# Kernel tuning notes

Measured on AMD Instinct MI355X. Metric: run time of the kernel, lower is better.

Reference implementation:

```python
import jax, jax.numpy as jnp
import numpy as np

N, E, D = 50000, 600000, 128
LN_EPS = 1e-5


def setup_inputs() -> dict:
    key = jax.random.key(0)
    ks = jax.random.split(key, 7)
    s = 1.0 / np.sqrt(D)
    x = jax.random.normal(ks[0], (N, D), dtype=jnp.float32)
    edge_index = jax.random.randint(ks[1], (2, E), 0, N, dtype=jnp.int32)
    Wq = jax.random.normal(ks[2], (D, D), dtype=jnp.float32) * s
    Wk = jax.random.normal(ks[3], (D, D), dtype=jnp.float32) * s
    Wv = jax.random.normal(ks[4], (D, D), dtype=jnp.float32) * s
    Wo = jax.random.normal(ks[5], (D, D), dtype=jnp.float32) * s
    bo = jnp.zeros((D,), dtype=jnp.float32)
    gamma = jnp.ones((D,), dtype=jnp.float32)
    beta = jnp.zeros((D,), dtype=jnp.float32)
    return {"x": x, "edge_index": edge_index, "Wq": Wq, "Wk": Wk,
            "Wv": Wv, "Wo": Wo, "bo": bo, "gamma": gamma, "beta": beta}


def reference(x, edge_index, Wq, Wk, Wv, Wo, bo, gamma, beta):
    src, dst = edge_index[0], edge_index[1]
    # gather endpoint features, project (torch Linear: y = x @ W.T)
    q = x[dst] @ Wq.T                      # [E, D]
    k = x[src] @ Wk.T                      # [E, D]
    v = x[src] @ Wv.T                      # [E, D]
    logits = jnp.sum(q * k, axis=-1, keepdims=True) / np.sqrt(D)  # [E, 1]
    msg = jax.nn.sigmoid(logits) * v       # [E, D]
    agg = jax.ops.segment_sum(msg, dst, num_segments=N)  # scatter-add -> [N, D]
    out = agg @ Wo.T + bo
    h = x + out
    # LayerNorm over last dim
    mu = jnp.mean(h, axis=-1, keepdims=True)
    var = jnp.mean(jnp.square(h - mu), axis=-1, keepdims=True)
    return (h - mu) * jax.lax.rsqrt(var + LN_EPS) * gamma + beta
```

## Files before the change

kernel.cpp:

```cpp
#include <hip/hip_runtime.h>
#include <math.h>


#define BM 64
#define QSCALE -0.08838834764831845f

typedef __attribute__((ext_vector_type(8))) short bfrag;
typedef __attribute__((ext_vector_type(4))) float f32x4;

__device__ __forceinline__ short f2bf(float f) {
    union { float f; unsigned u; } v; v.f = f;
    unsigned r = v.u + 0x7FFFu + ((v.u >> 16) & 1u);
    return (short)(r >> 16);
}
__device__ __forceinline__ float bf2f(short h) {
    union { unsigned u; float f; } v;
    v.u = ((unsigned)(unsigned short)h) << 16;
    return v.f;
}
__device__ __forceinline__ float klo(unsigned w) {
    union { unsigned u; float f; } v; v.u = w << 16; return v.f;
}
__device__ __forceinline__ float vhi(unsigned w) {
    union { unsigned u; float f; } v; v.u = w & 0xffff0000u; return v.f;
}

#define SWZ(x, pat) __int_as_float(__builtin_amdgcn_ds_swizzle(__float_as_int(x), pat))

__global__ __launch_bounds__(256) void zero_prep(
    const float* __restrict__ Wq, const float* __restrict__ Wk,
    const float* __restrict__ Wv, const float* __restrict__ Wo,
    short* __restrict__ whi, short* __restrict__ wlo,
    int* __restrict__ hist, int N)
{
    int g = blockIdx.x * 256 + threadIdx.x;
    if (g < N) hist[g] = 0;
    if (g < 65536) {
        const float* Ws[4] = {Wq, Wk, Wv, Wo};
        float f = Ws[g >> 14][g & 16383];
        short h = f2bf(f);
        short l = f2bf(f - bf2f(h));
        whi[g] = h; wlo[g] = l;
    }
}

__global__ __launch_bounds__(256) void qkv_mfma(
    const float* __restrict__ x,
    const short* __restrict__ whi, const short* __restrict__ wlo,
    float* __restrict__ Q, unsigned short* __restrict__ KV16, int N)
{
    __shared__ short xs_hi[64][136];
    __shared__ short xs_lo[64][136];

    const int tid = threadIdx.x;
    const int row0 = blockIdx.x * BM;

    #pragma unroll
    for (int i = 0; i < 8; ++i) {
        int idx = tid + 256 * i;
        int r = idx >> 5;
        int c4 = idx & 31;
        int gr = row0 + r;
        float4 val = make_float4(0.f, 0.f, 0.f, 0.f);
        if (gr < N) val = ((const float4*)(x + (size_t)gr * 128))[c4];
        short4 h, l;
        h.x = f2bf(val.x); l.x = f2bf(val.x - bf2f(h.x));
        h.y = f2bf(val.y); l.y = f2bf(val.y - bf2f(h.y));
        h.z = f2bf(val.z); l.z = f2bf(val.z - bf2f(h.z));
        h.w = f2bf(val.w); l.w = f2bf(val.w - bf2f(h.w));
        *((short4*)&xs_hi[r][c4 * 4]) = h;
        *((short4*)&xs_lo[r][c4 * 4]) = l;
    }
    __syncthreads();

    const int wid  = tid >> 6;
    const int lane = tid & 63;
    const int n16  = lane & 15;
    const int quad = lane >> 4;

    #pragma unroll 1
    for (int mat = 0; mat < 3; ++mat) {
        const short* __restrict__ WH = whi + mat * 16384;
        const short* __restrict__ WL = wlo + mat * 16384;
        const f32x4 zero = {0.f, 0.f, 0.f, 0.f};
        f32x4 acc[4][2];
        #pragma unroll
        for (int t = 0; t < 4; ++t) { acc[t][0] = zero; acc[t][1] = zero; }

        #pragma unroll
        for (int kc = 0; kc < 4; ++kc) {
            int k0 = kc * 32 + quad * 8;
            bfrag ah[4], al[4], bh[2], bl[2];
            #pragma unroll
            for (int t = 0; t < 4; ++t) {
                ah[t] = *((const bfrag*)&xs_hi[t * 16 + n16][k0]);
                al[t] = *((const bfrag*)&xs_lo[t * 16 + n16][k0]);
            }
            #pragma unroll
            for (int c = 0; c < 2; ++c) {
                int wr = (wid * 2 + c) * 16 + n16;
                bh[c] = *((const bfrag*)(WH + wr * 128 + k0));
                bl[c] = *((const bfrag*)(WL + wr * 128 + k0));
            }
            #pragma unroll
            for (int t = 0; t < 4; ++t)
                #pragma unroll
                for (int c = 0; c < 2; ++c) {
                    acc[t][c] = __builtin_amdgcn_mfma_f32_16x16x32_bf16(ah[t], bh[c], acc[t][c], 0, 0, 0);
                    acc[t][c] = __builtin_amdgcn_mfma_f32_16x16x32_bf16(al[t], bh[c], acc[t][c], 0, 0, 0);
                    acc[t][c] = __builtin_amdgcn_mfma_f32_16x16x32_bf16(ah[t], bl[c], acc[t][c], 0, 0, 0);
                }
        }
        #pragma unroll
        for (int t = 0; t < 4; ++t)
            #pragma unroll
            for (int r = 0; r < 4; ++r) {
                int grow = row0 + t * 16 + quad * 4 + r;
                if (grow < N) {
                    int c0 = (wid * 2 + 0) * 16 + n16;
                    int c1 = (wid * 2 + 1) * 16 + n16;
                    if (mat == 0) {
                        Q[(size_t)grow * 128 + c0] = acc[t][0][r] * QSCALE;
                        Q[(size_t)grow * 128 + c1] = acc[t][1][r] * QSCALE;
                    } else {
                        size_t base = (size_t)grow * 256 + (mat - 1);
                        KV16[base + 2 * c0] = (unsigned short)f2bf(acc[t][0][r]);
                        KV16[base + 2 * c1] = (unsigned short)f2bf(acc[t][1][r]);
                    }
                }
            }
    }
}

__global__ __launch_bounds__(256) void hist_kernel(
    const int* __restrict__ ei, int* __restrict__ hist, int E)
{
    int e = blockIdx.x * blockDim.x + threadIdx.x;
    if (e < E) atomicAdd(&hist[ei[E + e]], 1);
}

#define SCAN_TPB 256
#define SCAN_EPT 4

__global__ __launch_bounds__(SCAN_TPB) void scan_partial(
    const int* __restrict__ hist, int* __restrict__ offs,
    int* __restrict__ blockSums, int N)
{
    __shared__ int sdata[SCAN_TPB];
    int b = blockIdx.x;
    int t = threadIdx.x;
    int base = b * SCAN_TPB * SCAN_EPT + t * SCAN_EPT;
    int v[SCAN_EPT];
    int tot = 0;
    #pragma unroll
    for (int j = 0; j < SCAN_EPT; ++j) {
        int idx = base + j;
        v[j] = (idx < N) ? hist[idx] : 0;
        tot += v[j];
    }
    sdata[t] = tot;
    __syncthreads();
    for (int off = 1; off < SCAN_TPB; off <<= 1) {
        int xv = (t >= off) ? sdata[t - off] : 0;
        __syncthreads();
        sdata[t] += xv;
        __syncthreads();
    }
    int run = sdata[t] - tot;
    #pragma unroll
    for (int j = 0; j < SCAN_EPT; ++j) {
        int idx = base + j;
        if (idx < N) offs[idx] = run;
        run += v[j];
    }
    if (t == SCAN_TPB - 1) blockSums[b] = sdata[t];
}

__global__ __launch_bounds__(256) void scan_blocksums(int* __restrict__ blockSums, int nb)
{
    __shared__ int sdata[256];
    int t = threadIdx.x;
    int orig = (t < nb) ? blockSums[t] : 0;
    sdata[t] = orig;
    __syncthreads();
    for (int off = 1; off < 256; off <<= 1) {
        int xv = (t >= off) ? sdata[t - off] : 0;
        __syncthreads();
        sdata[t] += xv;
        __syncthreads();
    }
    if (t < nb) blockSums[t] = sdata[t] - orig;
}

__global__ __launch_bounds__(256) void scan_add(
    int* __restrict__ offs, int* __restrict__ starts,
    const int* __restrict__ blockSums, int N)
{
    int idx = blockIdx.x * blockDim.x + threadIdx.x;
    if (idx < N) {
        int vv = offs[idx] + blockSums[idx >> 10];
        offs[idx] = vv;
        starts[idx] = vv;
    }
}

__global__ __launch_bounds__(256) void scatter_kernel(
    const int* __restrict__ ei, int* __restrict__ offs,
    int* __restrict__ ssrc, int E)
{
    int e = blockIdx.x * blockDim.x + threadIdx.x;
    if (e < E) {
        int d = ei[E + e];
        int pos = atomicAdd(&offs[d], 1);
        ssrc[pos] = ei[e];
    }
}

__global__ __launch_bounds__(256) void node_agg(
    const int* __restrict__ ssrc,
    const int* __restrict__ starts,
    const int* __restrict__ endoffs,
    const float* __restrict__ Q, const unsigned short* __restrict__ KV16,
    float* __restrict__ agg, int N)
{
    int node = blockIdx.x * 4 + (threadIdx.x >> 6);
    if (node >= N) return;
    int lane = threadIdx.x & 63;
    int eg   = lane >> 4;
    int sl   = lane & 15;
    int start = starts[node];
    int end   = endoffs[node];

    const float4 q0 = *((const float4*)(Q + (size_t)node * 128 + sl * 8));
    const float4 q1 = *((const float4*)(Q + (size_t)node * 128 + sl * 8 + 4));

    float a0 = 0.f, a1 = 0.f, a2 = 0.f, a3 = 0.f;
    float a4 = 0.f, a5 = 0.f, a6 = 0.f, a7 = 0.f;

    const unsigned short* kvbase = KV16 + sl * 16;

    for (int i = start; i < end; i += 8) {
        int i0 = i + eg;
        int i1 = i + 4 + eg;
        int ok0 = (i0 < end);
        int ok1 = (i1 < end);
        i0 = ok0 ? i0 : (end - 1);
        i1 = ok1 ? i1 : (end - 1);
        int s0 = ssrc[i0];
        int s1 = ssrc[i1];
        const unsigned short* kp0 = kvbase + ((size_t)s0 << 8);
        const unsigned short* kp1 = kvbase + ((size_t)s1 << 8);
        uint4 wa0 = *((const uint4*)kp0);
        uint4 wa1 = *((const uint4*)(kp0 + 8));
        uint4 wb0 = *((const uint4*)kp1);
        uint4 wb1 = *((const uint4*)(kp1 + 8));

        float p0, p1;
        p0 = q0.x * klo(wa0.x);
        p0 = fmaf(q0.y, klo(wa0.y), p0);
        p0 = fmaf(q0.z, klo(wa0.z), p0);
        p0 = fmaf(q0.w, klo(wa0.w), p0);
        p0 = fmaf(q1.x, klo(wa1.x), p0);
        p0 = fmaf(q1.y, klo(wa1.y), p0);
        p0 = fmaf(q1.z, klo(wa1.z), p0);
        p0 = fmaf(q1.w, klo(wa1.w), p0);
        p1 = q0.x * klo(wb0.x);
        p1 = fmaf(q0.y, klo(wb0.y), p1);
        p1 = fmaf(q0.z, klo(wb0.z), p1);
        p1 = fmaf(q0.w, klo(wb0.w), p1);
        p1 = fmaf(q1.x, klo(wb1.x), p1);
        p1 = fmaf(q1.y, klo(wb1.y), p1);
        p1 = fmaf(q1.z, klo(wb1.z), p1);
        p1 = fmaf(q1.w, klo(wb1.w), p1);

        p0 += SWZ(p0, 0x041F); p1 += SWZ(p1, 0x041F);
        p0 += SWZ(p0, 0x081F); p1 += SWZ(p1, 0x081F);
        p0 += SWZ(p0, 0x101F); p1 += SWZ(p1, 0x101F);
        p0 += SWZ(p0, 0x201F); p1 += SWZ(p1, 0x201F);

        float c0 = __builtin_amdgcn_rcpf(1.f + __expf(p0));
        float c1 = __builtin_amdgcn_rcpf(1.f + __expf(p1));
        if (!ok0) c0 = 0.f;
        if (!ok1) c1 = 0.f;

        a0 = fmaf(c0, vhi(wa0.x), a0); a0 = fmaf(c1, vhi(wb0.x), a0);
        a1 = fmaf(c0, vhi(wa0.y), a1); a1 = fmaf(c1, vhi(wb0.y), a1);
        a2 = fmaf(c0, vhi(wa0.z), a2); a2 = fmaf(c1, vhi(wb0.z), a2);
        a3 = fmaf(c0, vhi(wa0.w), a3); a3 = fmaf(c1, vhi(wb0.w), a3);
        a4 = fmaf(c0, vhi(wa1.x), a4); a4 = fmaf(c1, vhi(wb1.x), a4);
        a5 = fmaf(c0, vhi(wa1.y), a5); a5 = fmaf(c1, vhi(wb1.y), a5);
        a6 = fmaf(c0, vhi(wa1.z), a6); a6 = fmaf(c1, vhi(wb1.z), a6);
        a7 = fmaf(c0, vhi(wa1.w), a7); a7 = fmaf(c1, vhi(wb1.w), a7);
    }

    a0 += SWZ(a0, 0x401F); a1 += SWZ(a1, 0x401F);
    a2 += SWZ(a2, 0x401F); a3 += SWZ(a3, 0x401F);
    a4 += SWZ(a4, 0x401F); a5 += SWZ(a5, 0x401F);
    a6 += SWZ(a6, 0x401F); a7 += SWZ(a7, 0x401F);
    a0 += __shfl_xor(a0, 32); a1 += __shfl_xor(a1, 32);
    a2 += __shfl_xor(a2, 32); a3 += __shfl_xor(a3, 32);
    a4 += __shfl_xor(a4, 32); a5 += __shfl_xor(a5, 32);
    a6 += __shfl_xor(a6, 32); a7 += __shfl_xor(a7, 32);

    if (eg == 0) {
        *((float4*)(agg + (size_t)node * 128 + sl * 8))     = make_float4(a0, a1, a2, a3);
        *((float4*)(agg + (size_t)node * 128 + sl * 8 + 4)) = make_float4(a4, a5, a6, a7);
    }
}

__global__ __launch_bounds__(256) void out_ln_mfma(
    const float* __restrict__ agg,
    const short* __restrict__ whi, const short* __restrict__ wlo,
    const float* __restrict__ bo, const float* __restrict__ x,
    const float* __restrict__ gamma, const float* __restrict__ beta,
    float* __restrict__ out, int N)
{
    __shared__ __align__(16) char smem[64 * 136 * 2 * 2];
    short (*xs_hi)[136] = (short(*)[136])smem;
    short (*xs_lo)[136] = (short(*)[136])(smem + 64 * 136 * 2);
    float (*hs)[132]    = (float(*)[132])smem;

    const int tid = threadIdx.x;
    const int row0 = blockIdx.x * BM;

    #pragma unroll
    for (int i = 0; i < 8; ++i) {
        int idx = tid + 256 * i;
        int r = idx >> 5;
        int c4 = idx & 31;
        int gr = row0 + r;
        float4 val = make_float4(0.f, 0.f, 0.f, 0.f);
        if (gr < N) val = ((const float4*)(agg + (size_t)gr * 128))[c4];
        short4 h, l;
        h.x = f2bf(val.x); l.x = f2bf(val.x - bf2f(h.x));
        h.y = f2bf(val.y); l.y = f2bf(val.y - bf2f(h.y));
        h.z = f2bf(val.z); l.z = f2bf(val.z - bf2f(h.z));
        h.w = f2bf(val.w); l.w = f2bf(val.w - bf2f(h.w));
        *((short4*)&xs_hi[r][c4 * 4]) = h;
        *((short4*)&xs_lo[r][c4 * 4]) = l;
    }
    __syncthreads();

    const int wid  = tid >> 6;
    const int lane = tid & 63;
    const int n16  = lane & 15;
    const int quad = lane >> 4;
    const short* __restrict__ WH = whi + 3 * 16384;
    const short* __restrict__ WL = wlo + 3 * 16384;

    const f32x4 zero = {0.f, 0.f, 0.f, 0.f};
    f32x4 acc[4][2];
    #pragma unroll
    for (int t = 0; t < 4; ++t) { acc[t][0] = zero; acc[t][1] = zero; }

    #pragma unroll
    for (int kc = 0; kc < 4; ++kc) {
        int k0 = kc * 32 + quad * 8;
        bfrag ah[4], al[4], bh[2], bl[2];
        #pragma unroll
        for (int t = 0; t < 4; ++t) {
            ah[t] = *((const bfrag*)&xs_hi[t * 16 + n16][k0]);
            al[t] = *((const bfrag*)&xs_lo[t * 16 + n16][k0]);
        }
        #pragma unroll
        for (int c = 0; c < 2; ++c) {
            int wr = (wid * 2 + c) * 16 + n16;
            bh[c] = *((const bfrag*)(WH + wr * 128 + k0));
            bl[c] = *((const bfrag*)(WL + wr * 128 + k0));
        }
        #pragma unroll
        for (int t = 0; t < 4; ++t)
            #pragma unroll
            for (int c = 0; c < 2; ++c) {
                acc[t][c] = __builtin_amdgcn_mfma_f32_16x16x32_bf16(ah[t], bh[c], acc[t][c], 0, 0, 0);
                acc[t][c] = __builtin_amdgcn_mfma_f32_16x16x32_bf16(al[t], bh[c], acc[t][c], 0, 0, 0);
                acc[t][c] = __builtin_amdgcn_mfma_f32_16x16x32_bf16(ah[t], bl[c], acc[t][c], 0, 0, 0);
            }
    }
    __syncthreads();

    #pragma unroll
    for (int t = 0; t < 4; ++t)
        #pragma unroll
        for (int r = 0; r < 4; ++r) {
            hs[t * 16 + quad * 4 + r][(wid * 2 + 0) * 16 + n16] = acc[t][0][r];
            hs[t * 16 + quad * 4 + r][(wid * 2 + 1) * 16 + n16] = acc[t][1][r];
        }
    __syncthreads();

    {
        int r = tid >> 2;
        int qd = tid & 3;
        int gr = row0 + r;
        float sum = 0.f, sq = 0.f;
        #pragma unroll
        for (int c = 0; c < 32; c += 4) {
            float4 g4 = *((float4*)&hs[r][qd * 32 + c]);
            float4 b4 = *((const float4*)(bo + qd * 32 + c));
            float4 x4 = make_float4(0.f, 0.f, 0.f, 0.f);
            if (gr < N) x4 = *((const float4*)(x + (size_t)gr * 128 + qd * 32 + c));
            float4 h = make_float4(g4.x + b4.x + x4.x, g4.y + b4.y + x4.y,
                                   g4.z + b4.z + x4.z, g4.w + b4.w + x4.w);
            *((float4*)&hs[r][qd * 32 + c]) = h;
            sum += h.x + h.y + h.z + h.w;
            sq += h.x * h.x + h.y * h.y + h.z * h.z + h.w * h.w;
        }
        sum += __shfl_xor(sum, 1); sum += __shfl_xor(sum, 2);
        sq  += __shfl_xor(sq, 1);  sq  += __shfl_xor(sq, 2);
        float mu = sum * (1.f / 128.f);
        float var = sq * (1.f / 128.f) - mu * mu;
        float rs = rsqrtf(var + 1e-5f);
        if (gr < N) {
            #pragma unroll
            for (int c = 0; c < 32; c += 4) {
                float4 h = *((float4*)&hs[r][qd * 32 + c]);
                float4 g = *((const float4*)(gamma + qd * 32 + c));
                float4 b = *((const float4*)(beta + qd * 32 + c));
                float4 o = make_float4((h.x - mu) * rs * g.x + b.x,
                                       (h.y - mu) * rs * g.y + b.y,
                                       (h.z - mu) * rs * g.z + b.z,
                                       (h.w - mu) * rs * g.w + b.w);
                *((float4*)(out + (size_t)gr * 128 + qd * 32 + c)) = o;
            }
        }
    }
}

extern "C" void kernel_launch(void* const* d_in, const int* in_sizes, int n_in,
                              void* d_out, int out_size, void* d_ws, size_t ws_size,
                              hipStream_t stream) {
    const float* x     = (const float*)d_in[0];
    const int*   ei    = (const int*)d_in[1];
    const float* Wq    = (const float*)d_in[2];
    const float* Wk    = (const float*)d_in[3];
    const float* Wv    = (const float*)d_in[4];
    const float* Wo    = (const float*)d_in[5];
    const float* bo    = (const float*)d_in[6];
    const float* gamma = (const float*)d_in[7];
    const float* beta  = (const float*)d_in[8];
    const int N = in_sizes[0] / 128;
    const int E = in_sizes[1] / 2;
    const size_t ND = (size_t)N * 128;

    float* ws  = (float*)d_ws;
    float* Q   = ws;
    unsigned short* KV16 = (unsigned short*)(Q + ND);
    float* agg = (float*)(KV16 + 2 * ND);
    int* hist      = (int*)(agg + ND);
    int* offs      = hist + N;
    int* starts    = offs + N;
    int* blockSums = starts + N;
    int* ssrc      = blockSums + 256;
    short* whi     = (short*)(ssrc + E);
    short* wlo     = whi + 4 * 16384;

    const int gzp = ((N > 65536 ? N : 65536) + 255) / 256;
    zero_prep<<<gzp, 256, 0, stream>>>(Wq, Wk, Wv, Wo, whi, wlo, hist, N);

    hist_kernel<<<(E + 255) / 256, 256, 0, stream>>>(ei, hist, E);
    const int nScanBlocks = (N + SCAN_TPB * SCAN_EPT - 1) / (SCAN_TPB * SCAN_EPT);
    scan_partial<<<nScanBlocks, SCAN_TPB, 0, stream>>>(hist, offs, blockSums, N);
    scan_blocksums<<<1, 256, 0, stream>>>(blockSums, nScanBlocks);
    scan_add<<<(N + 255) / 256, 256, 0, stream>>>(offs, starts, blockSums, N);
    scatter_kernel<<<(E + 255) / 256, 256, 0, stream>>>(ei, offs, ssrc, E);

    const int gq = (N + BM - 1) / BM;
    qkv_mfma<<<gq, 256, 0, stream>>>(x, whi, wlo, Q, KV16, N);

    node_agg<<<(N + 3) / 4, 256, 0, stream>>>(ssrc, starts, offs, Q, KV16, agg, N);

    out_ln_mfma<<<gq, 256, 0, stream>>>(agg, whi, wlo, bo, x, gamma, beta,
                                        (float*)d_out, N);
}
```

Measured before the change: 280.8 us.

## Store Q in bf16, fuse block-sum scan, prefetch next edge batch in aggregation

Result: faster. 268.2 us (-4.5%).

```diff
diff --git a/kernel.cpp b/kernel.cpp
--- a/kernel.cpp
+++ b/kernel.cpp
@@ -47,7 +47,7 @@
 __global__ __launch_bounds__(256) void qkv_mfma(
     const float* __restrict__ x,
     const short* __restrict__ whi, const short* __restrict__ wlo,
-    float* __restrict__ Q, unsigned short* __restrict__ KV16, int N)
+    unsigned short* __restrict__ Q16, unsigned short* __restrict__ KV16, int N)
 {
     __shared__ short xs_hi[64][136];
     __shared__ short xs_lo[64][136];
@@ -120,8 +120,8 @@
                     int c0 = (wid * 2 + 0) * 16 + n16;
                     int c1 = (wid * 2 + 1) * 16 + n16;
                     if (mat == 0) {
-                        Q[(size_t)grow * 128 + c0] = acc[t][0][r] * QSCALE;
-                        Q[(size_t)grow * 128 + c1] = acc[t][1][r] * QSCALE;
+                        Q16[(size_t)grow * 128 + c0] = (unsigned short)f2bf(acc[t][0][r] * QSCALE);
+                        Q16[(size_t)grow * 128 + c1] = (unsigned short)f2bf(acc[t][1][r] * QSCALE);
                     } else {
                         size_t base = (size_t)grow * 256 + (mat - 1);
                         KV16[base + 2 * c0] = (unsigned short)f2bf(acc[t][0][r]);
@@ -176,29 +176,27 @@
     if (t == SCAN_TPB - 1) blockSums[b] = sdata[t];
 }
 
-__global__ __launch_bounds__(256) void scan_blocksums(int* __restrict__ blockSums, int nb)
-{
-    __shared__ int sdata[256];
-    int t = threadIdx.x;
-    int orig = (t < nb) ? blockSums[t] : 0;
-    sdata[t] = orig;
-    __syncthreads();
-    for (int off = 1; off < 256; off <<= 1) {
-        int xv = (t >= off) ? sdata[t - off] : 0;
-        __syncthreads();
-        sdata[t] += xv;
-        __syncthreads();
-    }
-    if (t < nb) blockSums[t] = sdata[t] - orig;
-}
-
 __global__ __launch_bounds__(256) void scan_add(
     int* __restrict__ offs, int* __restrict__ starts,
-    const int* __restrict__ blockSums, int N)
-{
+    const int* __restrict__ blockSums, int N, int nb)
+{
+    __shared__ int bs[64];
+    int t = threadIdx.x;
+    if (t < 64) {
+        int v = (t < nb) ? blockSums[t] : 0;
+        #pragma unroll
+        for (int off = 1; off < 64; off <<= 1) {
+            int u = __shfl_up(v, off);
+            if (t >= off) v += u;
+        }
+        bs[t] = v;
+    }
+    __syncthreads();
     int idx = blockIdx.x * blockDim.x + threadIdx.x;
     if (idx < N) {
-        int vv = offs[idx] + blockSums[idx >> 10];
+        int blk = idx >> 10;
+        int pref = (blk == 0) ? 0 : bs[blk - 1];
+        int vv = offs[idx] + pref;
         offs[idx] = vv;
         starts[idx] = vv;
     }
@@ -220,7 +218,8 @@
     const int* __restrict__ ssrc,
     const int* __restrict__ starts,
     const int* __restrict__ endoffs,
-    const float* __restrict__ Q, const unsigned short* __restrict__ KV16,
+    const unsigned short* __restrict__ Q16,
+    const unsigned short* __restrict__ KV16,
     float* __restrict__ agg, int N)
 {
     int node = blockIdx.x * 4 + (threadIdx.x >> 6);
@@ -231,21 +230,27 @@
     int start = starts[node];
     int end   = endoffs[node];
 
-    const float4 q0 = *((const float4*)(Q + (size_t)node * 128 + sl * 8));
-    const float4 q1 = *((const float4*)(Q + (size_t)node * 128 + sl * 8 + 4));
+    if (start >= end) {
+        if (eg == 0) {
+            *((float4*)(agg + (size_t)node * 128 + sl * 8))     = make_float4(0.f, 0.f, 0.f, 0.f);
+            *((float4*)(agg + (size_t)node * 128 + sl * 8 + 4)) = make_float4(0.f, 0.f, 0.f, 0.f);
+        }
+        return;
+    }
+
+    bfrag qv = *((const bfrag*)(Q16 + (size_t)node * 128 + sl * 8));
+    float q0x = bf2f(qv[0]), q0y = bf2f(qv[1]), q0z = bf2f(qv[2]), q0w = bf2f(qv[3]);
+    float q1x = bf2f(qv[4]), q1y = bf2f(qv[5]), q1z = bf2f(qv[6]), q1w = bf2f(qv[7]);
 
     float a0 = 0.f, a1 = 0.f, a2 = 0.f, a3 = 0.f;
     float a4 = 0.f, a5 = 0.f, a6 = 0.f, a7 = 0.f;
 
     const unsigned short* kvbase = KV16 + sl * 16;
 
-    for (int i = start; i < end; i += 8) {
-        int i0 = i + eg;
-        int i1 = i + 4 + eg;
-        int ok0 = (i0 < end);
-        int ok1 = (i1 < end);
-        i0 = ok0 ? i0 : (end - 1);
-        i1 = ok1 ? i1 : (end - 1);
+    int i = start;
+    {
+        int i0 = i + eg;     i0 = (i0 < end) ? i0 : (end - 1);
+        int i1 = i + 4 + eg; i1 = (i1 < end) ? i1 : (end - 1);
         int s0 = ssrc[i0];
         int s1 = ssrc[i1];
         const unsigned short* kp0 = kvbase + ((size_t)s0 << 8);
@@ -255,42 +260,66 @@
         uint4 wb0 = *((const uint4*)kp1);
         uint4 wb1 = *((const uint4*)(kp1 + 8));
 
-        float p0, p1;
-        p0 = q0.x * klo(wa0.x);
-        p0 = fmaf(q0.y, klo(wa0.y), p0);
-        p0 = fmaf(q0.z, klo(wa0.z), p0);
-        p0 = fmaf(q0.w, klo(wa0.w), p0);
-        p0 = fmaf(q1.x, klo(wa1.x), p0);
-        p0 = fmaf(q1.y, klo(wa1.y), p0);
-        p0 = fmaf(q1.z, klo(wa1.z), p0);
-        p0 = fmaf(q1.w, klo(wa1.w), p0);
-        p1 = q0.x * klo(wb0.x);
-        p1 = fmaf(q0.y, klo(wb0.y), p1);
-        p1 = fmaf(q0.z, klo(wb0.z), p1);
-        p1 = fmaf(q0.w, klo(wb0.w), p1);
-        p1 = fmaf(q1.x, klo(wb1.x), p1);
-        p1 = fmaf(q1.y, klo(wb1.y), p1);
-        p1 = fmaf(q1.z, klo(wb1.z), p1);
-        p1 = fmaf(q1.w, klo(wb1.w), p1);
-
-        p0 += SWZ(p0, 0x041F); p1 += SWZ(p1, 0x041F);
-        p0 += SWZ(p0, 0x081F); p1 += SWZ(p1, 0x081F);
-        p0 += SWZ(p0, 0x101F); p1 += SWZ(p1, 0x101F);
-        p0 += SWZ(p0, 0x201F); p1 += SWZ(p1, 0x201F);
-
-        float c0 = __builtin_amdgcn_rcpf(1.f + __expf(p0));
-        float c1 = __builtin_amdgcn_rcpf(1.f + __expf(p1));
-        if (!ok0) c0 = 0.f;
-        if (!ok1) c1 = 0.f;
-
-        a0 = fmaf(c0, vhi(wa0.x), a0); a0 = fmaf(c1, vhi(wb0.x), a0);
-        a1 = fmaf(c0, vhi(wa0.y), a1); a1 = fmaf(c1, vhi(wb0.y), a1);
-        a2 = fmaf(c0, vhi(wa0.z), a2); a2 = fmaf(c1, vhi(wb0.z), a2);
-        a3 = fmaf(c0, vhi(wa0.w), a3); a3 = fmaf(c1, vhi(wb0.w), a3);
-        a4 = fmaf(c0, vhi(wa1.x), a4); a4 = fmaf(c1, vhi(wb1.x), a4);
-        a5 = fmaf(c0, vhi(wa1.y), a5); a5 = fmaf(c1, vhi(wb1.y), a5);
-        a6 = fmaf(c0, vhi(wa1.z), a6); a6 = fmaf(c1, vhi(wb1.z), a6);
-        a7 = fmaf(c0, vhi(wa1.w), a7); a7 = fmaf(c1, vhi(wb1.w), a7);
+        for (;;) {
+            bool more = (i + 8) < end;
+            uint4 na0, na1, nb0, nb1;
+            if (more) {
+                int j0 = i + 8 + eg;  j0 = (j0 < end) ? j0 : (end - 1);
+                int j1 = i + 12 + eg; j1 = (j1 < end) ? j1 : (end - 1);
+                int t0 = ssrc[j0];
+                int t1 = ssrc[j1];
+                const unsigned short* np0 = kvbase + ((size_t)t0 << 8);
+                const unsigned short* np1 = kvbase + ((size_t)t1 << 8);
+                na0 = *((const uint4*)np0);
+                na1 = *((const uint4*)(np0 + 8));
+                nb0 = *((const uint4*)np1);
+                nb1 = *((const uint4*)(np1 + 8));
+            }
+
+            int ok0 = ((i + eg) < end);
+            int ok1 = ((i + 4 + eg) < end);
+
+            float p0, p1;
+            p0 = q0x * klo(wa0.x);
+            p0 = fmaf(q0y, klo(wa0.y), p0);
+            p0 = fmaf(q0z, klo(wa0.z), p0);
+            p0 = fmaf(q0w, klo(wa0.w), p0);
+            p0 = fmaf(q1x, klo(wa1.x), p0);
+            p0 = fmaf(q1y, klo(wa1.y), p0);
+            p0 = fmaf(q1z, klo(wa1.z), p0);
+            p0 = fmaf(q1w, klo(wa1.w), p0);
+            p1 = q0x * klo(wb0.x);
+            p1 = fmaf(q0y, klo(wb0.y), p1);
+            p1 = fmaf(q0z, klo(wb0.z), p1);
+            p1 = fmaf(q0w, klo(wb0.w), p1);
+            p1 = fmaf(q1x, klo(wb1.x), p1);
+            p1 = fmaf(q1y, klo(wb1.y), p1);
+            p1 = fmaf(q1z, klo(wb1.z), p1);
+            p1 = fmaf(q1w, klo(wb1.w), p1);
+
+            p0 += SWZ(p0, 0x041F); p1 += SWZ(p1, 0x041F);
+            p0 += SWZ(p0, 0x081F); p1 += SWZ(p1, 0x081F);
+            p0 += SWZ(p0, 0x101F); p1 += SWZ(p1, 0x101F);
+            p0 += SWZ(p0, 0x201F); p1 += SWZ(p1, 0x201F);
+
+            float c0 = __builtin_amdgcn_rcpf(1.f + __expf(p0));
+            float c1 = __builtin_amdgcn_rcpf(1.f + __expf(p1));
+            if (!ok0) c0 = 0.f;
+            if (!ok1) c1 = 0.f;
+
+            a0 = fmaf(c0, vhi(wa0.x), a0); a0 = fmaf(c1, vhi(wb0.x), a0);
+            a1 = fmaf(c0, vhi(wa0.y), a1); a1 = fmaf(c1, vhi(wb0.y), a1);
+            a2 = fmaf(c0, vhi(wa0.z), a2); a2 = fmaf(c1, vhi(wb0.z), a2);
+            a3 = fmaf(c0, vhi(wa0.w), a3); a3 = fmaf(c1, vhi(wb0.w), a3);
+            a4 = fmaf(c0, vhi(wa1.x), a4); a4 = fmaf(c1, vhi(wb1.x), a4);
+            a5 = fmaf(c0, vhi(wa1.y), a5); a5 = fmaf(c1, vhi(wb1.y), a5);
+            a6 = fmaf(c0, vhi(wa1.z), a6); a6 = fmaf(c1, vhi(wb1.z), a6);
+            a7 = fmaf(c0, vhi(wa1.w), a7); a7 = fmaf(c1, vhi(wb1.w), a7);
+
+            if (!more) break;
+            wa0 = na0; wa1 = na1; wb0 = nb0; wb1 = nb1;
+            i += 8;
+        }
     }
 
     a0 += SWZ(a0, 0x401F); a1 += SWZ(a1, 0x401F);
@@ -442,9 +471,8 @@
     const int E = in_sizes[1] / 2;
     const size_t ND = (size_t)N * 128;
 
-    float* ws  = (float*)d_ws;
-    float* Q   = ws;
-    unsigned short* KV16 = (unsigned short*)(Q + ND);
+    unsigned short* Q16  = (unsigned short*)d_ws;
+    unsigned short* KV16 = Q16 + ND;
     float* agg = (float*)(KV16 + 2 * ND);
     int* hist      = (int*)(agg + ND);
     int* offs      = hist + N;
@@ -460,14 +488,13 @@
     hist_kernel<<<(E + 255) / 256, 256, 0, stream>>>(ei, hist, E);
     const int nScanBlocks = (N + SCAN_TPB * SCAN_EPT - 1) / (SCAN_TPB * SCAN_EPT);
     scan_partial<<<nScanBlocks, SCAN_TPB, 0, stream>>>(hist, offs, blockSums, N);
-    scan_blocksums<<<1, 256, 0, stream>>>(blockSums, nScanBlocks);
-    scan_add<<<(N + 255) / 256, 256, 0, stream>>>(offs, starts, blockSums, N);
+    scan_add<<<(N + 255) / 256, 256, 0, stream>>>(offs, starts, blockSums, N, nScanBlocks);
     scatter_kernel<<<(E + 255) / 256, 256, 0, stream>>>(ei, offs, ssrc, E);
 
     const int gq = (N + BM - 1) / BM;
-    qkv_mfma<<<gq, 256, 0, stream>>>(x, whi, wlo, Q, KV16, N);
-
-    node_agg<<<(N + 3) / 4, 256, 0, stream>>>(ssrc, starts, offs, Q, KV16, agg, N);
+    qkv_mfma<<<gq, 256, 0, stream>>>(x, whi, wlo, Q16, KV16, N);
+
+    node_agg<<<(N + 3) / 4, 256, 0, stream>>>(ssrc, starts, offs, Q16, KV16, agg, N);
 
     out_ln_mfma<<<gq, 256, 0, stream>>>(agg, whi, wlo, bo, x, gamma, beta,
                                         (float*)d_out, N);
```
